# Optimization experiments

Measured on AMD Instinct MI355X. Metric: run time of the kernel, lower is better.

The kernel has to match this reference:

```python
import jax, jax.numpy as jnp
import numpy as np

N = 50000        # nodes
R = 51           # enriched relations (25 fwd + 25 inverse + self-loop)
F_IN = 32        # feat_size
E = 32           # embed_size
C = 16           # num_classes
B = 30           # num_bases
NNZ = 2_000_000  # nonzeros in vertical adjacency


def _xavier(key, shape):
    # mimics nn.init.xavier_uniform_ with gain for relu (sqrt(2))
    fan_in, fan_out = shape[-2], shape[-1]
    a = np.sqrt(2.0) * np.sqrt(6.0 / (fan_in + fan_out))
    return jax.random.uniform(key, shape, jnp.float32, -a, a)


def setup_inputs() -> dict:
    key = jax.random.key(0)
    ks = jax.random.split(key, 8)
    # COO of vertical adjacency, shape (R*N, N)
    rows = jax.random.randint(ks[0], (NNZ,), 0, R * N)
    cols = jax.random.randint(ks[1], (NNZ,), 0, N)
    # row-normalized values: vals = 1 / row_degree  (sum_sparse with rows=True)
    deg = jax.ops.segment_sum(jnp.ones((NNZ,), jnp.float32), rows, num_segments=R * N)
    vals = (1.0 / jnp.maximum(deg, 1.0))[rows]
    features = jax.random.normal(ks[2], (N, F_IN), jnp.float32)
    comps1 = _xavier(ks[3], (R, B))
    bases1 = _xavier(ks[4], (B, F_IN, E))
    comps2 = _xavier(ks[5], (R, B))
    bases2 = _xavier(ks[6], (B, E, C))
    bias1 = jnp.zeros((E,), jnp.float32)
    bias2 = jnp.zeros((C,), jnp.float32)
    return {
        "features": features, "vals": vals,
        "comps1": comps1, "bases1": bases1, "bias1": bias1,
        "comps2": comps2, "bases2": bases2, "bias2": bias2,
        "rows": rows, "cols": cols,
    }


def _spmm(rows, cols, vals, x):
    # (R*N, N) sparse @ (N, f) dense -> (R*N, f)
    return jax.ops.segment_sum(vals[:, None] * x[cols], rows, num_segments=R * N)


def reference(features, vals, comps1, bases1, bias1, comps2, bases2, bias2, rows, cols):
    # layer 1: SpMM then basis-decomposed per-relation mixing
    h = _spmm(rows, cols, vals, features).reshape(R, N, F_IN)   # (r, n, f)
    w1 = jnp.einsum('rb,bfe->rfe', comps1, bases1)              # (r, f, e)
    h = jnp.einsum('rnf,rfe->ne', h, w1)                        # (n, e)
    h = jax.nn.relu(h + bias1)
    # layer 2
    h = _spmm(rows, cols, vals, h).reshape(R, N, E)             # (r, n, e)
    w2 = jnp.einsum('rb,bho->rho', comps2, bases2)              # (r, e, c)
    h = jnp.einsum('rho,rnh->no', w2, h)                        # (n, c)
    return h + bias2
```

## Files before the change

kernel.cpp:

```cpp
#include <hip/hip_runtime.h>

#define NNODES 50000
#define RREL 51
#define FIN 32
#define EDIM 32
#define CDIM 16
#define BB 30
#define NNZ_ 2000000
#define EPB 4096
#define NBUK 391
#define PCAP_MAX 2750128

typedef unsigned int uint32;
typedef unsigned short ushort;
typedef uint32 u32x2 __attribute__((ext_vector_type(2)));
typedef uint32 u32x4 __attribute__((ext_vector_type(4)));
typedef short bf16x8 __attribute__((ext_vector_type(8)));
typedef float f32x4 __attribute__((ext_vector_type(4)));
typedef float f32x16 __attribute__((ext_vector_type(16)));

static __device__ __forceinline__ uint32 pack_bf16x2(float a, float b) {
    uint32 ua = __builtin_bit_cast(uint32, a);
    uint32 ub = __builtin_bit_cast(uint32, b);
    ua += 0x7fffu + ((ua >> 16) & 1u);
    ub += 0x7fffu + ((ub >> 16) & 1u);
    return (ua >> 16) | (ub & 0xffff0000u);
}
static __device__ __forceinline__ ushort bf16_1(float x) {
    uint32 u = __builtin_bit_cast(uint32, x);
    u += 0x7fffu + ((u >> 16) & 1u);
    return (ushort)(u >> 16);
}

__global__ void k_weights2(const float* __restrict__ bases1, const float* __restrict__ bases2,
                           ushort* __restrict__ Wb1, ushort* __restrict__ Wb2) {
    int i = blockIdx.x * 256 + threadIdx.x;
    if (i < 960 * 32) {
        int e = i & 31, k = i >> 5;
        int b = k >> 5, f = k & 31;
        float v = bases1[b * 1024 + f * 32 + e];
        Wb1[((k >> 3) * 32 + e) * 8 + (k & 7)] = bf16_1(v);
    }
    if (i < 960 * 16) {
        int e = i & 15, k = i >> 4;
        int b = k >> 5, h = k & 31;
        float v = bases2[b * 512 + h * 16 + e];
        Wb2[((k >> 3) * 16 + e) * 8 + (k & 7)] = bf16_1(v);
    }
}

__global__ void k_tobf16(const float2* __restrict__ src, uint32* __restrict__ dst, int n2) {
    int i = blockIdx.x * 256 + threadIdx.x;
    if (i < n2) {
        float2 f = src[i];
        dst[i] = pack_bf16x2(f.x, f.y);
    }
}

__global__ __launch_bounds__(1024) void k_bukhist(const int* __restrict__ rows,
                                                  int* __restrict__ buk_cnt) {
    __shared__ int lc[NBUK];
    int t = threadIdx.x;
    if (t < NBUK) lc[t] = 0;
    __syncthreads();
    size_t k = (size_t)blockIdx.x * EPB + (size_t)t * 4;
    int rr[4];
    if (k + 4 <= NNZ_) {
        int4 rw = *(const int4*)(rows + k);
        rr[0] = rw.x; rr[1] = rw.y; rr[2] = rw.z; rr[3] = rw.w;
    } else {
#pragma unroll
        for (int j = 0; j < 4; j++) rr[j] = (k + j < NNZ_) ? rows[k + j] : -1;
    }
#pragma unroll
    for (int j = 0; j < 4; j++)
        if (rr[j] >= 0) {
            int rel = rr[j] / NNODES;
            int dst = rr[j] - rel * NNODES;
            atomicAdd(&lc[dst >> 7], 1);
        }
    __syncthreads();
    if (t < NBUK) atomicAdd(&buk_cnt[t], lc[t]);
}

__global__ void k_scan1(const int* __restrict__ buk_cnt, int* __restrict__ buk_base,
                        int* __restrict__ buk_cur) {
    if (threadIdx.x == 0) {
        int a = 0;
        for (int b = 0; b < NBUK; b++) { buk_base[b] = a; buk_cur[b] = a; a += buk_cnt[b]; }
        buk_base[NBUK] = a;
    }
}

__global__ __launch_bounds__(1024) void k_bucket2(const int* __restrict__ rows,
                                                  const int* __restrict__ cols,
                                                  const float* __restrict__ vals,
                                                  int* __restrict__ buk_cur,
                                                  u32x2* __restrict__ tok8,
                                                  float* __restrict__ sval_b) {
    __shared__ int bukc[NBUK], lb[NBUK], gb[NBUK];
    __shared__ int ssum[1024];
    __shared__ u32x2 st8[EPB];
    __shared__ float sv[EPB];
    int t = threadIdx.x;
    size_t base = (size_t)blockIdx.x * EPB;
    int total = (int)(((size_t)NNZ_ - base < (size_t)EPB) ? ((size_t)NNZ_ - base) : (size_t)EPB);
    if (t < NBUK) bukc[t] = 0;
    __syncthreads();
    size_t k = base + (size_t)t * 4;
    int bv[4]; uint32 tx[4], ty[4]; float vv[4];
    if (k + 4 <= NNZ_) {
        int4 rw = *(const int4*)(rows + k);
        int4 cw = *(const int4*)(cols + k);
        float4 vw = *(const float4*)(vals + k);
        int rr[4] = {rw.x, rw.y, rw.z, rw.w};
        int cc[4] = {cw.x, cw.y, cw.z, cw.w};
        vv[0] = vw.x; vv[1] = vw.y; vv[2] = vw.z; vv[3] = vw.w;
#pragma unroll
        for (int j = 0; j < 4; j++) {
            int rel = rr[j] / NNODES;
            int dst = rr[j] - rel * NNODES;
            bv[j] = dst >> 7;
            tx[j] = (uint32)dst | ((uint32)rel << 16);
            ty[j] = (uint32)cc[j] | ((uint32)rel << 16);
        }
    } else {
#pragma unroll
        for (int j = 0; j < 4; j++) {
            if (k + j < NNZ_) {
                int r = rows[k + j];
                int rel = r / NNODES;
                int dst = r - rel * NNODES;
                bv[j] = dst >> 7;
                tx[j] = (uint32)dst | ((uint32)rel << 16);
                ty[j] = (uint32)cols[k + j] | ((uint32)rel << 16);
                vv[j] = vals[k + j];
            } else bv[j] = -1;
        }
    }
#pragma unroll
    for (int j = 0; j < 4; j++)
        if (bv[j] >= 0) atomicAdd(&bukc[bv[j]], 1);
    __syncthreads();
    int v = (t < NBUK) ? bukc[t] : 0;
    ssum[t] = v;
    __syncthreads();
    for (int off = 1; off < 1024; off <<= 1) {
        int u = (t >= off) ? ssum[t - off] : 0;
        __syncthreads();
        ssum[t] += u;
        __syncthreads();
    }
    if (t < NBUK) { lb[t] = ssum[t] - v; gb[t] = atomicAdd(&buk_cur[t], v); }
    __syncthreads();
    if (t < NBUK) bukc[t] = 0;
    __syncthreads();
#pragma unroll
    for (int j = 0; j < 4; j++) {
        if (bv[j] >= 0) {
            int slot = lb[bv[j]] + atomicAdd(&bukc[bv[j]], 1);
            u32x2 w; w.x = tx[j]; w.y = ty[j];
            st8[slot] = w;
            sv[slot] = vv[j];
        }
    }
    __syncthreads();
    for (int s = t; s < total; s += 1024) {
        u32x2 w = st8[s];
        int bk = (int)((w.x & 0xFFFFu) >> 7);
        int pos = gb[bk] + (s - lb[bk]);
        tok8[pos] = w;
        sval_b[pos] = sv[s];
    }
}

__global__ __launch_bounds__(256) void k_rank3a(const u32x2* __restrict__ tok8,
                                                const int* __restrict__ buk_base,
                                                int* __restrict__ pbuk_cnt) {
    __shared__ int lcnt[128];
    __shared__ int tot;
    int b = blockIdx.x, t = threadIdx.x;
    if (t < 128) lcnt[t] = 0;
    if (t == 0) tot = 0;
    __syncthreads();
    int lo = buk_base[b], hi = buk_base[b + 1];
    for (int i = lo + t; i < hi; i += 256) atomicAdd(&lcnt[tok8[i].x & 127], 1);
    __syncthreads();
    if (t < 128) atomicAdd(&tot, (lcnt[t] + 15) & ~15);
    __syncthreads();
    if (t == 0) pbuk_cnt[b] = tot;
}

__global__ void k_scan2(const int* __restrict__ pbuk_cnt, int* __restrict__ pbuk_base) {
    if (threadIdx.x == 0) {
        int a = 0;
        for (int b = 0; b < NBUK; b++) { pbuk_base[b] = a; a += pbuk_cnt[b]; }
        pbuk_base[NBUK] = a;
    }
}

__global__ __launch_bounds__(256) void k_place(const u32x2* __restrict__ tok8,
                                               const float* __restrict__ sval_b,
                                               const int* __restrict__ buk_base,
                                               const int* __restrict__ pbuk_base,
                                               int* __restrict__ pdst_base,
                                               uint32* __restrict__ pe_sr,
                                               float* __restrict__ pe_val) {
    __shared__ int lcnt[128], lexc[128], lrank[128], ssc[128];
    int b = blockIdx.x, t = threadIdx.x;
    int lo = buk_base[b], hi = buk_base[b + 1], pb = pbuk_base[b];
    if (t < 128) { lcnt[t] = 0; lrank[t] = 0; }
    __syncthreads();
    for (int i = lo + t; i < hi; i += 256) atomicAdd(&lcnt[tok8[i].x & 127], 1);
    __syncthreads();
    int v = 0;
    if (t < 128) { v = (lcnt[t] + 15) & ~15; ssc[t] = v; }
    __syncthreads();
    for (int off = 1; off < 128; off <<= 1) {
        int u = (t >= off && t < 128) ? ssc[t - off] : 0;
        __syncthreads();
        if (t < 128) ssc[t] += u;
        __syncthreads();
    }
    if (t < 128) {
        lexc[t] = ssc[t] - v;
        int d = (b << 7) + t;
        if (d <= NNODES) pdst_base[d] = pb + lexc[t];
    }
    __syncthreads();
    for (int i = lo + t; i < hi; i += 256) {
        u32x2 w = tok8[i];
        int dl = (int)(w.x & 127u);
        int pos = pb + lexc[dl] + atomicAdd(&lrank[dl], 1);
        pe_sr[pos] = w.y;
        pe_val[pos] = sval_b[i];
    }
    if (t < 128) {
        int s0 = pb + lexc[t] + lcnt[t];
        int s1 = pb + lexc[t] + ((lcnt[t] + 15) & ~15);
        for (int i = s0; i < s1; i++) { pe_sr[i] = 0u; pe_val[i] = 0.f; }
    }
}

template <int FO, bool RELU, bool BF16OUT>
__global__ __launch_bounds__(256) void k_fused(const uint32* __restrict__ pe_sr,
                                               const float* __restrict__ pe_val,
                                               const int* __restrict__ pdst_base,
                                               const u32x4* __restrict__ Xb,
                                               const u32x4* __restrict__ Wb,
                                               const float* __restrict__ comps,
                                               const float* __restrict__ bias,
                                               void* __restrict__ outp) {
    __shared__ ushort comps_lb[RREL * 32];
    __shared__ uint32 eds[4][64];
    __shared__ float edv[4][64];
    __shared__ __align__(16) ushort xst[4][4][512];
    __shared__ __align__(16) ushort ubuf[4][4][968];
    int t = threadIdx.x, lane = t & 63, wv = t >> 6;
    for (int i = t; i < RREL * 32; i += 256) {
        int r = i >> 5, b = i & 31;
        comps_lb[i] = (b < BB) ? bf16_1(comps[r * BB + b]) : (ushort)0;
    }
    __syncthreads();
    int m = lane & 31, hf = lane >> 5, k0 = hf * 8;
    int ln15 = lane & 15, quad = lane >> 4;
    int d0 = (blockIdx.x * 4 + wv) * 8;
    if (d0 >= NNODES) return;
    uint32 pvs = __builtin_nontemporal_load(&pe_sr[pdst_base[d0] + lane]);
    float  pvv = __builtin_nontemporal_load(&pe_val[pdst_base[d0] + lane]);
#pragma unroll 1
    for (int batch = 0; batch < 2; batch++) {
        int db = d0 + batch * 4;
#pragma unroll 1
        for (int s = 0; s < 4; s++) {
            int d = db + s;
            int lo = pdst_base[d], segEnd = pdst_base[d + 1];
            f32x16 acc;
#pragma unroll
            for (int i = 0; i < 16; i++) acc[i] = 0.f;
#pragma unroll 1
            for (int c0 = lo; c0 < segEnd; c0 += 64) {
                eds[wv][lane] = pvs;
                edv[wv][lane] = pvv;
                int nxt = c0 + 64; if (nxt > segEnd) nxt = segEnd;
                pvs = __builtin_nontemporal_load(&pe_sr[nxt + lane]);
                pvv = __builtin_nontemporal_load(&pe_val[nxt + lane]);
                int nwin = (segEnd - c0) >> 4;
                if (nwin > 4) nwin = 4;
#pragma unroll 1
                for (int wi = 0; wi < nwin; wi++) {
                    int src = (int)(eds[wv][wi * 16 + (lane >> 2)] & 0xFFFFu);
                    u32x4 xv = Xb[(size_t)src * 4 + (lane & 3)];
                    *(u32x4*)&xst[wv][wi][lane * 8] = xv;
                }
#pragma unroll 1
                for (int wi = 0; wi < nwin; wi++) {
                    const ushort* xs = &xst[wv][wi][0];
                    uint32 bw0, bw1, bw2, bw3;
                    {
                        uint32 a0 = xs[(k0 + 0) * 32 + m], a1 = xs[(k0 + 1) * 32 + m];
                        uint32 a2 = xs[(k0 + 2) * 32 + m], a3 = xs[(k0 + 3) * 32 + m];
                        uint32 a4 = xs[(k0 + 4) * 32 + m], a5 = xs[(k0 + 5) * 32 + m];
                        uint32 a6 = xs[(k0 + 6) * 32 + m], a7 = xs[(k0 + 7) * 32 + m];
                        bw0 = a0 | (a1 << 16); bw1 = a2 | (a3 << 16);
                        bw2 = a4 | (a5 << 16); bw3 = a6 | (a7 << 16);
                    }
                    u32x4 bvq = { bw0, bw1, bw2, bw3 };
                    float cc[8];
#pragma unroll
                    for (int j = 0; j < 8; j++) {
                        uint32 sr = eds[wv][wi * 16 + k0 + j];
                        float vv = edv[wv][wi * 16 + k0 + j];
                        uint32 cu = (uint32)comps_lb[((sr >> 16) << 5) | m] << 16;
                        cc[j] = vv * __builtin_bit_cast(float, cu);
                    }
                    u32x4 avq = { pack_bf16x2(cc[0], cc[1]), pack_bf16x2(cc[2], cc[3]),
                                  pack_bf16x2(cc[4], cc[5]), pack_bf16x2(cc[6], cc[7]) };
                    acc = __builtin_amdgcn_mfma_f32_32x32x16_bf16(
                        __builtin_bit_cast(bf16x8, avq), __builtin_bit_cast(bf16x8, bvq),
                        acc, 0, 0, 0);
                }
            }
#pragma unroll
            for (int r = 0; r < 16; r++) {
                int b = (r & 3) + 8 * (r >> 2) + 4 * hf;
                float vme = acc[r];
                float vot = __shfl_xor(vme, 1, 64);
                if (b < BB && !(m & 1)) {
                    *(uint32*)&ubuf[wv][s][b * 32 + m] = pack_bf16x2(vme, vot);
                }
            }
        }
        const int NT = FO / 16;
        f32x4 a2[NT];
#pragma unroll
        for (int tt = 0; tt < NT; tt++)
#pragma unroll
            for (int i = 0; i < 4; i++) a2[tt][i] = 0.f;
#pragma unroll 6
        for (int ks = 0; ks < 30; ks++) {
            bf16x8 af = *(const bf16x8*)&ubuf[wv][ln15 & 3][ks * 32 + quad * 8];
#pragma unroll
            for (int tt = 0; tt < NT; tt++) {
                bf16x8 bf2 = __builtin_bit_cast(bf16x8, Wb[(ks * 4 + quad) * FO + ln15 + 16 * tt]);
                a2[tt] = __builtin_amdgcn_mfma_f32_16x16x32_bf16(af, bf2, a2[tt], 0, 0, 0);
            }
        }
        if (quad == 0) {
#pragma unroll
            for (int r = 0; r < 4; r++) {
                int dst = db + r;
                if (dst < NNODES) {
                    if (BF16OUT) {
                        ushort* hp = (ushort*)outp;
#pragma unroll
                        for (int tt = 0; tt < NT; tt++) {
                            float o = a2[tt][r] + bias[ln15 + 16 * tt];
                            if (RELU) o = fmaxf(o, 0.f);
                            hp[(size_t)dst * FO + ln15 + 16 * tt] = bf16_1(o);
                        }
                    } else {
                        float o = a2[0][r] + bias[ln15];
                        if (RELU) o = fmaxf(o, 0.f);
                        ((float*)outp)[(size_t)dst * FO + ln15] = o;
                    }
                }
            }
        }
    }
}

extern "C" void kernel_launch(void* const* d_in, const int* in_sizes, int n_in,
                              void* d_out, int out_size, void* d_ws, size_t ws_size,
                              hipStream_t stream) {
    const float* features = (const float*)d_in[0];
    const float* vals     = (const float*)d_in[1];
    const float* comps1   = (const float*)d_in[2];
    const float* bases1   = (const float*)d_in[3];
    const float* bias1    = (const float*)d_in[4];
    const float* comps2   = (const float*)d_in[5];
    const float* bases2   = (const float*)d_in[6];
    const float* bias2    = (const float*)d_in[7];
    const int*   rows     = (const int*)d_in[8];
    const int*   cols     = (const int*)d_in[9];
    float* out = (float*)d_out;

    float* ws = (float*)d_ws;
    size_t o = 0;
    ushort* Wb1 = (ushort*)(ws + o); o += 960 * 32 / 2;
    ushort* Wb2 = (ushort*)(ws + o); o += 960 * 16 / 2;
    uint32* Xb  = (uint32*)(ws + o); o += (size_t)NNODES * 16;
    uint32* h1b = (uint32*)(ws + o); o += (size_t)NNODES * 16;
    uint32* pe_sr  = (uint32*)(ws + o); o += PCAP_MAX;
    float*  pe_val = (float*)(ws + o);  o += PCAP_MAX;
    int* pdst_base = (int*)(ws + o); o += NNODES + 8;
    int* buk_cnt   = (int*)(ws + o); o += NBUK;
    int* buk_base  = (int*)(ws + o); o += NBUK + 1;
    int* buk_cur   = (int*)(ws + o); o += NBUK;
    int* pbuk_cnt  = (int*)(ws + o); o += NBUK;
    int* pbuk_base = (int*)(ws + o); o += NBUK + 1;
    o = (o + 1) & ~(size_t)1;
    u32x2* tok8 = (u32x2*)(ws + o); o += 2 * (size_t)NNZ_;
    float* sval_b = (float*)(ws + o); o += (size_t)NNZ_;

    const int NB = (NNZ_ + EPB - 1) / EPB;

    hipMemsetAsync(buk_cnt, 0, NBUK * sizeof(int), stream);

    k_weights2<<<(960 * 32 + 255) / 256, 256, 0, stream>>>(bases1, bases2, Wb1, Wb2);
    k_tobf16<<<(NNODES * FIN / 2 + 255) / 256, 256, 0, stream>>>((const float2*)features, Xb,
                                                                 NNODES * FIN / 2);
    k_bukhist<<<NB, 1024, 0, stream>>>(rows, buk_cnt);
    k_scan1<<<1, 64, 0, stream>>>(buk_cnt, buk_base, buk_cur);
    k_bucket2<<<NB, 1024, 0, stream>>>(rows, cols, vals, buk_cur, tok8, sval_b);
    k_rank3a<<<NBUK, 256, 0, stream>>>(tok8, buk_base, pbuk_cnt);
    k_scan2<<<1, 64, 0, stream>>>(pbuk_cnt, pbuk_base);
    k_place<<<NBUK, 256, 0, stream>>>(tok8, sval_b, buk_base, pbuk_base, pdst_base, pe_sr, pe_val);

    k_fused<EDIM, true, true><<<(NNODES + 31) / 32, 256, 0, stream>>>(
        pe_sr, pe_val, pdst_base, (const u32x4*)Xb, (const u32x4*)Wb1, comps1, bias1, h1b);
    k_fused<CDIM, false, false><<<(NNODES + 31) / 32, 256, 0, stream>>>(
        pe_sr, pe_val, pdst_base, (const u32x4*)h1b, (const u32x4*)Wb2, comps2, bias2, out);
}
```

Baseline: 383.9 us.

## Prefetch next chunk's gathered source rows into registers during MFMA windows

The per-chunk X row gather is moved out of the compute loop. The gather for the next 64-edge chunk is now issued right after the current chunk's MFMAs, using shuffles of the prefetched edge indices, so global gather latency overlaps the next iteration's LDS staging and coefficient preparation. The window loops are manually unrolled to four conditional steps, and the coefficient packing is hoisted ahead of the LDS stores. This adds 16 VGPRs of gather buffers, which may lower occupancy, and issues gathers for all four windows even when fewer are valid, relying on padded edge arrays.

```diff
diff --git a/kernel.cpp b/kernel.cpp
--- a/kernel.cpp
+++ b/kernel.cpp
@@ -266,8 +266,46 @@
     int ln15 = lane & 15, quad = lane >> 4;
     int d0 = (blockIdx.x * 4 + wv) * 8;
     if (d0 >= NNODES) return;
-    uint32 pvs = __builtin_nontemporal_load(&pe_sr[pdst_base[d0] + lane]);
-    float  pvv = __builtin_nontemporal_load(&pe_val[pdst_base[d0] + lane]);
+
+    auto ccprep = [&](int wi) -> u32x4 {
+        float cc[8];
+#pragma unroll
+        for (int j = 0; j < 8; j++) {
+            uint32 sr = eds[wv][wi * 16 + k0 + j];
+            float vv = edv[wv][wi * 16 + k0 + j];
+            uint32 cu = (uint32)comps_lb[((sr >> 16) << 5) | m] << 16;
+            cc[j] = vv * __builtin_bit_cast(float, cu);
+        }
+        u32x4 r = { pack_bf16x2(cc[0], cc[1]), pack_bf16x2(cc[2], cc[3]),
+                    pack_bf16x2(cc[4], cc[5]), pack_bf16x2(cc[6], cc[7]) };
+        return r;
+    };
+    auto dowin = [&](int wi, u32x4 avq, f32x16 a) -> f32x16 {
+        const ushort* xs = &xst[wv][wi][0];
+        uint32 b0 = (uint32)xs[(k0 + 0) * 32 + m] | ((uint32)xs[(k0 + 1) * 32 + m] << 16);
+        uint32 b1 = (uint32)xs[(k0 + 2) * 32 + m] | ((uint32)xs[(k0 + 3) * 32 + m] << 16);
+        uint32 b2 = (uint32)xs[(k0 + 4) * 32 + m] | ((uint32)xs[(k0 + 5) * 32 + m] << 16);
+        uint32 b3 = (uint32)xs[(k0 + 6) * 32 + m] | ((uint32)xs[(k0 + 7) * 32 + m] << 16);
+        u32x4 bvq = { b0, b1, b2, b3 };
+        return __builtin_amdgcn_mfma_f32_32x32x16_bf16(
+            __builtin_bit_cast(bf16x8, avq), __builtin_bit_cast(bf16x8, bvq), a, 0, 0, 0);
+    };
+
+    int base0 = pdst_base[d0];
+    uint32 pvs = __builtin_nontemporal_load(&pe_sr[base0 + lane]);
+    float  pvv = __builtin_nontemporal_load(&pe_val[base0 + lane]);
+    u32x4 gx0, gx1, gx2, gx3;
+    {
+        int s0_ = __shfl((int)pvs, (lane >> 2), 64);
+        gx0 = Xb[(size_t)((uint32)s0_ & 0xFFFFu) * 4 + (lane & 3)];
+        int s1_ = __shfl((int)pvs, 16 + (lane >> 2), 64);
+        gx1 = Xb[(size_t)((uint32)s1_ & 0xFFFFu) * 4 + (lane & 3)];
+        int s2_ = __shfl((int)pvs, 32 + (lane >> 2), 64);
+        gx2 = Xb[(size_t)((uint32)s2_ & 0xFFFFu) * 4 + (lane & 3)];
+        int s3_ = __shfl((int)pvs, 48 + (lane >> 2), 64);
+        gx3 = Xb[(size_t)((uint32)s3_ & 0xFFFFu) * 4 + (lane & 3)];
+    }
+
 #pragma unroll 1
     for (int batch = 0; batch < 2; batch++) {
         int db = d0 + batch * 4;
@@ -283,43 +321,34 @@
                 eds[wv][lane] = pvs;
                 edv[wv][lane] = pvv;
                 int nxt = c0 + 64; if (nxt > segEnd) nxt = segEnd;
-                pvs = __builtin_nontemporal_load(&pe_sr[nxt + lane]);
-                pvv = __builtin_nontemporal_load(&pe_val[nxt + lane]);
+                uint32 npvs = __builtin_nontemporal_load(&pe_sr[nxt + lane]);
+                float  npvv = __builtin_nontemporal_load(&pe_val[nxt + lane]);
                 int nwin = (segEnd - c0) >> 4;
                 if (nwin > 4) nwin = 4;
-#pragma unroll 1
-                for (int wi = 0; wi < nwin; wi++) {
-                    int src = (int)(eds[wv][wi * 16 + (lane >> 2)] & 0xFFFFu);
-                    u32x4 xv = Xb[(size_t)src * 4 + (lane & 3)];
-                    *(u32x4*)&xst[wv][wi][lane * 8] = xv;
+                u32x4 av0, av1, av2, av3;
+                av0 = ccprep(0);
+                if (nwin > 1) av1 = ccprep(1);
+                if (nwin > 2) av2 = ccprep(2);
+                if (nwin > 3) av3 = ccprep(3);
+                *(u32x4*)&xst[wv][0][lane * 8] = gx0;
+                if (nwin > 1) *(u32x4*)&xst[wv][1][lane * 8] = gx1;
+                if (nwin > 2) *(u32x4*)&xst[wv][2][lane * 8] = gx2;
+                if (nwin > 3) *(u32x4*)&xst[wv][3][lane * 8] = gx3;
+                acc = dowin(0, av0, acc);
+                if (nwin > 1) acc = dowin(1, av1, acc);
+                if (nwin > 2) acc = dowin(2, av2, acc);
+                if (nwin > 3) acc = dowin(3, av3, acc);
+                {
+                    int s0_ = __shfl((int)npvs, (lane >> 2), 64);
+                    gx0 = Xb[(size_t)((uint32)s0_ & 0xFFFFu) * 4 + (lane & 3)];
+                    int s1_ = __shfl((int)npvs, 16 + (lane >> 2), 64);
+                    gx1 = Xb[(size_t)((uint32)s1_ & 0xFFFFu) * 4 + (lane & 3)];
+                    int s2_ = __shfl((int)npvs, 32 + (lane >> 2), 64);
+                    gx2 = Xb[(size_t)((uint32)s2_ & 0xFFFFu) * 4 + (lane & 3)];
+                    int s3_ = __shfl((int)npvs, 48 + (lane >> 2), 64);
+                    gx3 = Xb[(size_t)((uint32)s3_ & 0xFFFFu) * 4 + (lane & 3)];
                 }
-#pragma unroll 1
-                for (int wi = 0; wi < nwin; wi++) {
-                    const ushort* xs = &xst[wv][wi][0];
-                    uint32 bw0, bw1, bw2, bw3;
-                    {
-                        uint32 a0 = xs[(k0 + 0) * 32 + m], a1 = xs[(k0 + 1) * 32 + m];
-                        uint32 a2 = xs[(k0 + 2) * 32 + m], a3 = xs[(k0 + 3) * 32 + m];
-                        uint32 a4 = xs[(k0 + 4) * 32 + m], a5 = xs[(k0 + 5) * 32 + m];
-                        uint32 a6 = xs[(k0 + 6) * 32 + m], a7 = xs[(k0 + 7) * 32 + m];
-                        bw0 = a0 | (a1 << 16); bw1 = a2 | (a3 << 16);
-                        bw2 = a4 | (a5 << 16); bw3 = a6 | (a7 << 16);
-                    }
-                    u32x4 bvq = { bw0, bw1, bw2, bw3 };
-                    float cc[8];
-#pragma unroll
-                    for (int j = 0; j < 8; j++) {
-                        uint32 sr = eds[wv][wi * 16 + k0 + j];
-                        float vv = edv[wv][wi * 16 + k0 + j];
-                        uint32 cu = (uint32)comps_lb[((sr >> 16) << 5) | m] << 16;
-                        cc[j] = vv * __builtin_bit_cast(float, cu);
-                    }
-                    u32x4 avq = { pack_bf16x2(cc[0], cc[1]), pack_bf16x2(cc[2], cc[3]),
-                                  pack_bf16x2(cc[4], cc[5]), pack_bf16x2(cc[6], cc[7]) };
-                    acc = __builtin_amdgcn_mfma_f32_32x32x16_bf16(
-                        __builtin_bit_cast(bf16x8, avq), __builtin_bit_cast(bf16x8, bvq),
-                        acc, 0, 0, 0);
-                }
+                pvs = npvs; pvv = npvv;
             }
 #pragma unroll
             for (int r = 0; r < 16; r++) {
```

New measurement: 361.2 us. -5.9%, faster.
